# Optimization experiments

Measured on AMD Instinct MI355X. Metric: run time of the kernel, lower is better.

## Reference

```python
import jax, jax.numpy as jnp
import numpy as np

H = 2048      # hidden_size
DM = 4096     # intermediate_size
N = 16        # ssm state size
K = 4         # conv kernel
R = 128       # time_step_rank
B_SZ = 1
L = 1024


def setup_inputs() -> dict:
    key = jax.random.key(0)
    ks = jax.random.split(key, 10)
    s = 0.02
    hidden_states = jax.random.normal(ks[0], (B_SZ, L, H), dtype=jnp.float32)
    W_in = jax.random.normal(ks[1], (2 * DM, H), dtype=jnp.float32) * s
    conv_w = jax.random.normal(ks[2], (DM, 1, K), dtype=jnp.float32) * 0.3
    conv_b = jax.random.normal(ks[3], (DM,), dtype=jnp.float32) * 0.1
    W_x = jax.random.normal(ks[4], (R + 2 * N, DM), dtype=jnp.float32) * s
    W_dt = jax.random.normal(ks[5], (DM, R), dtype=jnp.float32) * s
    b_dt = jax.random.normal(ks[6], (DM,), dtype=jnp.float32) * 0.1
    # A_log init: log(arange(1..N)) broadcast over channels (per __init__)
    A_log = jnp.broadcast_to(jnp.log(jnp.arange(1, N + 1, dtype=jnp.float32))[None, :], (DM, N)).copy()
    D_param = jnp.ones((DM,), dtype=jnp.float32)
    W_out = jax.random.normal(ks[7], (H, DM), dtype=jnp.float32) * s
    return {"hidden_states": hidden_states, "W_in": W_in, "conv_w": conv_w,
            "conv_b": conv_b, "W_x": W_x, "W_dt": W_dt, "b_dt": b_dt,
            "A_log": A_log, "D_param": D_param, "W_out": W_out}


def reference(hidden_states, W_in, conv_w, conv_b, W_x, W_dt, b_dt, A_log, D_param, W_out):
    # in_proj then chunk into hidden / gate (torch chunks dim=1 after transpose)
    proj = hidden_states @ W_in.T                     # [B, L, 2D]
    h, gate = proj[..., :DM], proj[..., DM:]          # each [B, L, D]
    # depthwise causal conv1d, padding K-1 then truncate to L (left-pad == same)
    h_cl = jnp.transpose(h, (0, 2, 1))                # [B, D, L]
    hc = jax.lax.conv_general_dilated(
        h_cl, conv_w, window_strides=(1,), padding=[(K - 1, 0)],
        dimension_numbers=("NCH", "OIH", "NCH"), feature_group_count=DM)
    hc = jax.nn.silu(hc + conv_b[None, :, None])      # [B, D, L]
    hc_ld = jnp.transpose(hc, (0, 2, 1))              # [B, L, D]
    # x_proj -> dt, B, C
    ssm_p = hc_ld @ W_x.T                             # [B, L, R+2N]
    ts, Bm, Cm = ssm_p[..., :R], ssm_p[..., R:R + N], ssm_p[..., R + N:]
    dt = jax.nn.softplus(ts @ W_dt.T + b_dt)          # [B, L, D]
    A = -jnp.exp(A_log)                               # [D, N]
    dA = jnp.exp(dt[:, :, :, None] * A[None, None, :, :])            # [B, L, D, N]
    dBu = dt[:, :, :, None] * Bm[:, :, None, :] * hc_ld[:, :, :, None]  # [B, L, D, N]
    # selective scan over time: state = dA*state + dBu; y = <state, C>
    def step(state, inp):
        dA_t, dBu_t, C_t = inp                        # [B,D,N],[B,D,N],[B,N]
        state = dA_t * state + dBu_t
        y = jnp.einsum("bdn,bn->bd", state, C_t)
        return state, y
    init = jnp.zeros((hidden_states.shape[0], DM, N), dtype=hidden_states.dtype)
    _, ys = jax.lax.scan(step, init,
                         (jnp.swapaxes(dA, 0, 1), jnp.swapaxes(dBu, 0, 1), jnp.swapaxes(Cm, 0, 1)))
    y = jnp.transpose(ys, (1, 0, 2))                  # [B, L, D]
    y = y + hc_ld * D_param[None, None, :]            # skip via D
    y = y * jax.nn.silu(gate)                         # gating
    return y @ W_out.T                                # [B, L, H]
```

## Files before the change

### kernel.cpp

```cpp
#include <hip/hip_runtime.h>
#include <math.h>

#define AS1 __attribute__((address_space(1)))
#define AS3 __attribute__((address_space(3)))

typedef __attribute__((ext_vector_type(8))) short short8;
typedef __attribute__((ext_vector_type(4))) float f32x4;

static __device__ __forceinline__ unsigned short f2bf(float f) {
    unsigned u = __float_as_uint(f);
    unsigned r = (u + 0x7fffu + ((u >> 16) & 1u)) >> 16;
    return (unsigned short)r;
}

__global__ __launch_bounds__(256) void cvt_f32_bf16(const float* __restrict__ src,
                                                    unsigned short* __restrict__ dst,
                                                    int n4) {
    int i = blockIdx.x * 256 + threadIdx.x;
    int stride = gridDim.x * 256;
    for (; i < n4; i += stride) {
        float4 v = ((const float4*)src)[i];
        ushort4 o;
        o.x = f2bf(v.x); o.y = f2bf(v.y); o.z = f2bf(v.z); o.w = f2bf(v.w);
        ((ushort4*)dst)[i] = o;
    }
}

__global__ __launch_bounds__(256) void cvt_ts(const float* __restrict__ ssmp,
                                              unsigned short* __restrict__ ts) {
    int i = blockIdx.x * 256 + threadIdx.x;
    int t = i >> 5, c4 = (i & 31) * 4;
    float4 v = *(const float4*)&ssmp[t * 160 + c4];
    ushort4 o;
    o.x = f2bf(v.x); o.y = f2bf(v.y); o.z = f2bf(v.z); o.w = f2bf(v.w);
    *(ushort4*)&ts[t * 128 + c4] = o;
}

__global__ __launch_bounds__(256) void conv_silu(const float* __restrict__ h,
                                                 const float* __restrict__ cw,
                                                 const float* __restrict__ cb,
                                                 float* __restrict__ hc_f,
                                                 unsigned short* __restrict__ hc_bf) {
    int idx = blockIdx.x * 256 + threadIdx.x;
    int d = idx & 4095, t = idx >> 12;
    float acc = cb[d];
    float4 w = *(const float4*)&cw[d * 4];
    const float* wp = (const float*)&w;
#pragma unroll
    for (int k = 0; k < 4; ++k) {
        int tt = t + k - 3;
        if (tt >= 0) acc += h[tt * 4096 + d] * wp[k];
    }
    float s = acc / (1.f + __expf(-acc));
    hc_f[idx] = s;
    hc_bf[idx] = f2bf(s);
}

enum { EPI_PLAIN = 0, EPI_SPLIT = 1, EPI_ATOMIC = 2, EPI_SOFTPLUS = 3 };

template <int BM, int EPI>
__global__ __launch_bounds__(256)
void gemm_bt(const short* __restrict__ A, const short* __restrict__ B,
             float* __restrict__ C, float* __restrict__ C2,
             const float* __restrict__ bias,
             int M, int N, int K, int ldc, int kcLen) {
    __shared__ short A_lds[BM * 32];
    __shared__ short B_lds[128 * 32];
    const int tid = threadIdx.x;
    const int wv = tid >> 6, ln = tid & 63;
    const int lr = ln & 15, kg = ln >> 4;
    const int m0 = blockIdx.y * BM;
    const int n0 = blockIdx.x * 128;
    const int kbeg = blockIdx.z * kcLen;
    const int kend = kbeg + kcLen;
    const int wm = wv >> 1, wn = wv & 1;
    constexpr int MR = BM / 32;

    f32x4 acc[MR][4];
#pragma unroll
    for (int mi = 0; mi < MR; ++mi)
#pragma unroll
        for (int ni = 0; ni < 4; ++ni) acc[mi][ni] = (f32x4){0.f, 0.f, 0.f, 0.f};

    const int arow = tid >> 2;
    const int kq8 = (tid & 3) * 8;

    for (int k0 = kbeg; k0 < kend; k0 += 32) {
#pragma unroll
        for (int r = 0; r < BM / 64; ++r) {
            const short* srcA = A + (size_t)(m0 + r * 64 + arow) * K + (k0 + kq8);
            short* dstA = &A_lds[(r * 64 + wv * 16) * 32];
            __builtin_amdgcn_global_load_lds((const AS1 void*)srcA, (AS3 void*)dstA, 16, 0, 0);
        }
#pragma unroll
        for (int r = 0; r < 2; ++r) {
            int brow = n0 + r * 64 + arow;
            if (brow > N - 1) brow = N - 1;
            const short* srcB = B + (size_t)brow * K + (k0 + kq8);
            short* dstB = &B_lds[(r * 64 + wv * 16) * 32];
            __builtin_amdgcn_global_load_lds((const AS1 void*)srcB, (AS3 void*)dstB, 16, 0, 0);
        }
        __syncthreads();

        short8 av[MR], bv[4];
#pragma unroll
        for (int mi = 0; mi < MR; ++mi)
            av[mi] = *(const short8*)&A_lds[(wm * (BM / 2) + mi * 16 + lr) * 32 + kg * 8];
#pragma unroll
        for (int ni = 0; ni < 4; ++ni)
            bv[ni] = *(const short8*)&B_lds[(wn * 64 + ni * 16 + lr) * 32 + kg * 8];
#pragma unroll
        for (int mi = 0; mi < MR; ++mi)
#pragma unroll
            for (int ni = 0; ni < 4; ++ni)
                acc[mi][ni] = __builtin_amdgcn_mfma_f32_16x16x32_bf16(av[mi], bv[ni], acc[mi][ni], 0, 0, 0);
        __syncthreads();
    }

#pragma unroll
    for (int mi = 0; mi < MR; ++mi) {
        int crow0 = m0 + wm * (BM / 2) + mi * 16 + kg * 4;
#pragma unroll
        for (int ni = 0; ni < 4; ++ni) {
            int ccol = n0 + wn * 64 + ni * 16 + lr;
#pragma unroll
            for (int i = 0; i < 4; ++i) {
                float v = acc[mi][ni][i];
                size_t crow = (size_t)(crow0 + i);
                if constexpr (EPI == EPI_PLAIN) {
                    C[crow * ldc + ccol] = v;
                } else if constexpr (EPI == EPI_SPLIT) {
                    if (ccol < 4096) C[crow * 4096 + ccol] = v;
                    else C2[crow * 4096 + (ccol - 4096)] = v;
                } else if constexpr (EPI == EPI_ATOMIC) {
                    if (ccol < N) atomicAdd(&C[crow * ldc + ccol], v);
                } else {
                    float x = v + bias[ccol];
                    C[crow * ldc + ccol] = fmaxf(x, 0.f) + log1pf(__expf(-fabsf(x)));
                }
            }
        }
    }
}

#define CLEN 16
#define NCH 64

__global__ __launch_bounds__(256)
void scan_p1(const float* __restrict__ dt, const float* __restrict__ hc,
             const float* __restrict__ ssmp, const float* __restrict__ A_log,
             float* __restrict__ Sbuf, float* __restrict__ dtsum) {
    const int tid = threadIdx.x;
    const int c = blockIdx.x & (NCH - 1);
    const int db = blockIdx.x >> 6;
    const int d = db * 256 + tid;
    const int t0 = c * CLEN;

    float Ac[16];
#pragma unroll
    for (int i = 0; i < 4; ++i) {
        float4 v = *(const float4*)&A_log[d * 16 + i * 4];
        Ac[i*4+0] = -__expf(v.x); Ac[i*4+1] = -__expf(v.y);
        Ac[i*4+2] = -__expf(v.z); Ac[i*4+3] = -__expf(v.w);
    }

    __shared__ float sB[CLEN][16];
    sB[tid >> 4][tid & 15] = ssmp[(t0 + (tid >> 4)) * 160 + 128 + (tid & 15)];
    __syncthreads();

    float st[16];
#pragma unroll
    for (int n = 0; n < 16; ++n) st[n] = 0.f;
    float ds = 0.f;

    for (int tt = 0; tt < CLEN; ++tt) {
        float dtv = dt[(size_t)(t0 + tt) * 4096 + d];
        float hcv = hc[(size_t)(t0 + tt) * 4096 + d];
        float du = dtv * hcv;
        ds += dtv;
#pragma unroll
        for (int n = 0; n < 16; ++n) {
            float dA = __expf(dtv * Ac[n]);
            st[n] = fmaf(dA, st[n], du * sB[tt][n]);
        }
    }

    float* o = Sbuf + ((size_t)c * 4096 + d) * 16;
#pragma unroll
    for (int i = 0; i < 4; ++i)
        *(float4*)&o[i * 4] = make_float4(st[i*4], st[i*4+1], st[i*4+2], st[i*4+3]);
    dtsum[c * 4096 + d] = ds;
}

__global__ __launch_bounds__(256)
void scan_p2(const float* __restrict__ A_log, const float* __restrict__ dtsum,
             float* __restrict__ S) {
    const int idx = blockIdx.x * 256 + threadIdx.x;
    const int d = idx >> 4;
    const float Ac = -__expf(A_log[idx]);
    float s = 0.f;
    for (int c = 0; c < NCH; ++c) {
        size_t o = (size_t)c * 65536 + idx;
        float sl = S[o];
        float P = __expf(Ac * dtsum[c * 4096 + d]);
        S[o] = s;
        s = fmaf(P, s, sl);
    }
}

__global__ __launch_bounds__(256)
void scan_p3(const float* __restrict__ dt, const float* __restrict__ hc,
             const float* __restrict__ ssmp, const float* __restrict__ A_log,
             const float* __restrict__ Dp, const float* __restrict__ gate,
             const float* __restrict__ Sinit, unsigned short* __restrict__ y_bf) {
    const int tid = threadIdx.x;
    const int c = blockIdx.x & (NCH - 1);
    const int db = blockIdx.x >> 6;
    const int d = db * 256 + tid;
    const int t0 = c * CLEN;

    float Ac[16];
#pragma unroll
    for (int i = 0; i < 4; ++i) {
        float4 v = *(const float4*)&A_log[d * 16 + i * 4];
        Ac[i*4+0] = -__expf(v.x); Ac[i*4+1] = -__expf(v.y);
        Ac[i*4+2] = -__expf(v.z); Ac[i*4+3] = -__expf(v.w);
    }
    const float Dcoef = Dp[d];

    __shared__ float sB[CLEN][16], sC[CLEN][16];
    {
        int tt = tid >> 4, nn = tid & 15;
        sB[tt][nn] = ssmp[(t0 + tt) * 160 + 128 + nn];
        sC[tt][nn] = ssmp[(t0 + tt) * 160 + 144 + nn];
    }
    __syncthreads();

    float st[16];
    {
        const float* si = Sinit + ((size_t)c * 4096 + d) * 16;
#pragma unroll
        for (int i = 0; i < 4; ++i) {
            float4 v = *(const float4*)&si[i * 4];
            st[i*4] = v.x; st[i*4+1] = v.y; st[i*4+2] = v.z; st[i*4+3] = v.w;
        }
    }

    for (int tt = 0; tt < CLEN; ++tt) {
        size_t g = (size_t)(t0 + tt) * 4096 + d;
        float dtv = dt[g];
        float hcv = hc[g];
        float du = dtv * hcv;
        float p[16];
#pragma unroll
        for (int n = 0; n < 16; ++n) {
            float dA = __expf(dtv * Ac[n]);
            st[n] = fmaf(dA, st[n], du * sB[tt][n]);
            p[n] = st[n] * sC[tt][n];
        }
#pragma unroll
        for (int n = 0; n < 8; ++n) p[n] += p[n + 8];
#pragma unroll
        for (int n = 0; n < 4; ++n) p[n] += p[n + 4];
        p[0] += p[2]; p[1] += p[3];
        float csum = p[0] + p[1];
        float gv = gate[g];
        float yv = (csum + hcv * Dcoef) * (gv / (1.f + __expf(-gv)));
        y_bf[g] = f2bf(yv);
    }
}

extern "C" void kernel_launch(void* const* d_in, const int* in_sizes, int n_in,
                              void* d_out, int out_size, void* d_ws, size_t ws_size,
                              hipStream_t stream) {
    (void)in_sizes; (void)n_in; (void)out_size; (void)ws_size;
    const float* hidden = (const float*)d_in[0];
    const float* W_in   = (const float*)d_in[1];
    const float* conv_w = (const float*)d_in[2];
    const float* conv_b = (const float*)d_in[3];
    const float* W_x    = (const float*)d_in[4];
    const float* W_dt   = (const float*)d_in[5];
    const float* b_dt   = (const float*)d_in[6];
    const float* A_log  = (const float*)d_in[7];
    const float* D_p    = (const float*)d_in[8];
    const float* W_out  = (const float*)d_in[9];
    float* out = (float*)d_out;

    char* w = (char*)d_ws;
    unsigned short* hid_bf = (unsigned short*)w;  w += (size_t)1024 * 2048 * 2;
    unsigned short* Wbig   = (unsigned short*)w;  w += (size_t)8192 * 2048 * 2;
    float* h_buf           = (float*)w;           w += (size_t)1024 * 4096 * 4;
    float* gate            = (float*)w;           w += (size_t)1024 * 4096 * 4;
    float* hc_f            = (float*)w;           w += (size_t)1024 * 4096 * 4;
    unsigned short* hc_bf  = (unsigned short*)w;  w += (size_t)1024 * 4096 * 2;
    float* ssmp            = (float*)w;           w += (size_t)1024 * 160 * 4;
    unsigned short* ts_bf  = (unsigned short*)w;  w += (size_t)1024 * 128 * 2;
    unsigned short* Wx_bf  = (unsigned short*)w;  w += (size_t)160 * 4096 * 2;
    unsigned short* Wdt_bf = (unsigned short*)w;  w += (size_t)4096 * 128 * 2;
    unsigned short* y_bf   = (unsigned short*)w;  w += (size_t)1024 * 4096 * 2;
    float* Sbuf            = (float*)w;           w += (size_t)NCH * 4096 * 16 * 4;
    float* dtsum           = (float*)w;           w += (size_t)NCH * 4096 * 4;

    hipMemsetAsync(ssmp, 0, (size_t)1024 * 160 * 4, stream);

    cvt_f32_bf16<<<2048, 256, 0, stream>>>(hidden, hid_bf, 1024 * 2048 / 4);
    cvt_f32_bf16<<<4096, 256, 0, stream>>>(W_in, Wbig, 8192 * 2048 / 4);
    cvt_f32_bf16<<<640, 256, 0, stream>>>(W_x, Wx_bf, 160 * 4096 / 4);
    cvt_f32_bf16<<<512, 256, 0, stream>>>(W_dt, Wdt_bf, 4096 * 128 / 4);

    gemm_bt<128, EPI_SPLIT><<<dim3(64, 8, 1), 256, 0, stream>>>(
        (const short*)hid_bf, (const short*)Wbig, h_buf, gate, nullptr,
        1024, 8192, 2048, 8192, 2048);

    conv_silu<<<16384, 256, 0, stream>>>(h_buf, conv_w, conv_b, hc_f, hc_bf);

    cvt_f32_bf16<<<2048, 256, 0, stream>>>(W_out, Wbig, 2048 * 4096 / 4);

    gemm_bt<128, EPI_ATOMIC><<<dim3(2, 8, 16), 256, 0, stream>>>(
        (const short*)hc_bf, (const short*)Wx_bf, ssmp, nullptr, nullptr,
        1024, 160, 4096, 160, 256);

    cvt_ts<<<128, 256, 0, stream>>>(ssmp, ts_bf);

    gemm_bt<128, EPI_SOFTPLUS><<<dim3(32, 8, 1), 256, 0, stream>>>(
        (const short*)ts_bf, (const short*)Wdt_bf, h_buf, nullptr, b_dt,
        1024, 4096, 128, 4096, 128);

    scan_p1<<<NCH * 16, 256, 0, stream>>>(h_buf, hc_f, ssmp, A_log, Sbuf, dtsum);
    scan_p2<<<256, 256, 0, stream>>>(A_log, dtsum, Sbuf);
    scan_p3<<<NCH * 16, 256, 0, stream>>>(h_buf, hc_f, ssmp, A_log, D_p, gate, Sbuf, y_bf);

    gemm_bt<64, EPI_PLAIN><<<dim3(16, 16, 1), 256, 0, stream>>>(
        (const short*)y_bf, (const short*)Wbig, out, nullptr, nullptr,
        1024, 2048, 4096, 2048, 4096);
}
```

Baseline: 269.7 us.

## Replace in_proj GEMM with 512-thread 128x256 tile double-buffered LDS kernel

Swaps the in_proj GEMM for a new kernel that uses 8 waves per block, a 128x256 output tile with BK=64, and async global_load_lds into double-buffered, XOR-swizzled LDS. Block IDs are remapped so neighbouring blocks share panels in L2. The aim is more operand reuse per block and overlapping global loads with MFMA work. In exchange it needs more LDS and registers, allowing at most 2 blocks per CU, and an unused three-stage variant is left in the file.

Measured after the change: 252.0 us. -6.5%, faster.

```diff
diff --git a/kernel.cpp b/kernel.cpp
--- a/kernel.cpp
+++ b/kernel.cpp
@@ -6,6 +6,9 @@
 
 typedef __attribute__((ext_vector_type(8))) short short8;
 typedef __attribute__((ext_vector_type(4))) float f32x4;
+
+#define WAITV(n) asm volatile("s_waitcnt vmcnt(" #n ")" ::: "memory")
+#define BARRIER() asm volatile("s_barrier" ::: "memory")
 
 static __device__ __forceinline__ unsigned short f2bf(float f) {
     unsigned u = __float_as_uint(f);
@@ -54,6 +57,224 @@
     float s = acc / (1.f + __expf(-acc));
     hc_f[idx] = s;
     hc_bf[idx] = f2bf(s);
+}
+
+__global__ __launch_bounds__(512, 2)
+void gemm8p_split(const short* __restrict__ A, const short* __restrict__ B,
+                  float* __restrict__ C0, float* __restrict__ C1,
+                  int M, int N, int K) {
+    __shared__ short lds[2 * 24576];
+
+    const int tid = threadIdx.x;
+    const int wv = tid >> 6, ln = tid & 63;
+    const int lr = ln & 15, kg = ln >> 4;
+    const int wm = wv >> 2, wn = wv & 3;
+
+    const int bid = blockIdx.x;
+    const int swz = (bid & 7) * 32 + (bid >> 3);
+    const int by = swz & 7, bx = swz >> 3;
+    const int m0 = by * 128;
+    const int n0 = bx * 256;
+    const int NT = K >> 6;
+
+    f32x4 acc[4][4];
+#pragma unroll
+    for (int mi = 0; mi < 4; ++mi)
+#pragma unroll
+        for (int ni = 0; ni < 4; ++ni) acc[mi][ni] = (f32x4){0.f, 0.f, 0.f, 0.f};
+
+    const short* Abase = A + (size_t)m0 * K;
+    const short* Bbase = B + (size_t)n0 * K;
+
+#define STAGE(kt, b)                                                          \
+    {                                                                         \
+        short* lbase = &lds[(b) * 24576];                                     \
+        _Pragma("unroll")                                                     \
+        for (int r = 0; r < 2; ++r) {                                         \
+            int c = r * 512 + tid;                                            \
+            int row = c >> 3, cb8 = (c & 7) << 4;                             \
+            int scb = cb8 ^ ((row & 7) << 4);                                 \
+            const short* src = Abase + (size_t)row * K + (kt) * 64 + (scb >> 1); \
+            short* dst = lbase + (r * 512 + wv * 64) * 8;                     \
+            __builtin_amdgcn_global_load_lds((const AS1 void*)src,            \
+                                             (AS3 void*)dst, 16, 0, 0);       \
+        }                                                                     \
+        _Pragma("unroll")                                                     \
+        for (int r = 0; r < 4; ++r) {                                         \
+            int c = r * 512 + tid;                                            \
+            int row = c >> 3, cb8 = (c & 7) << 4;                             \
+            int scb = cb8 ^ ((row & 7) << 4);                                 \
+            const short* src = Bbase + (size_t)row * K + (kt) * 64 + (scb >> 1); \
+            short* dst = lbase + 8192 + (r * 512 + wv * 64) * 8;              \
+            __builtin_amdgcn_global_load_lds((const AS1 void*)src,            \
+                                             (AS3 void*)dst, 16, 0, 0);       \
+        }                                                                     \
+    }
+
+    STAGE(0, 0);
+    if (NT > 1) STAGE(1, 1);
+
+    for (int kt = 0; kt < NT; ++kt) {
+        const int b = kt & 1;
+        if (kt + 2 < NT) STAGE(kt + 2, b);
+        if (kt + 1 < NT) { WAITV(6); } else { WAITV(0); }
+        BARRIER();
+        {
+            const short* la = &lds[b * 24576];
+            const short* lb = la + 8192;
+#pragma unroll
+            for (int ks = 0; ks < 2; ++ks) {
+                short8 av[4], bv[4];
+#pragma unroll
+                for (int mi = 0; mi < 4; ++mi) {
+                    int row = wm * 64 + mi * 16 + lr;
+                    int col = (ks * 32 + kg * 8) ^ ((row & 7) << 3);
+                    av[mi] = *(const short8*)&la[row * 64 + col];
+                }
+#pragma unroll
+                for (int ni = 0; ni < 4; ++ni) {
+                    int row = wn * 64 + ni * 16 + lr;
+                    int col = (ks * 32 + kg * 8) ^ ((row & 7) << 3);
+                    bv[ni] = *(const short8*)&lb[row * 64 + col];
+                }
+                __builtin_amdgcn_s_setprio(1);
+#pragma unroll
+                for (int mi = 0; mi < 4; ++mi)
+#pragma unroll
+                    for (int ni = 0; ni < 4; ++ni)
+                        acc[mi][ni] = __builtin_amdgcn_mfma_f32_16x16x32_bf16(
+                            av[mi], bv[ni], acc[mi][ni], 0, 0, 0);
+                __builtin_amdgcn_s_setprio(0);
+            }
+        }
+        BARRIER();
+    }
+#undef STAGE
+
+#pragma unroll
+    for (int mi = 0; mi < 4; ++mi) {
+        int crow0 = m0 + wm * 64 + mi * 16 + kg * 4;
+#pragma unroll
+        for (int ni = 0; ni < 4; ++ni) {
+            int ccol = n0 + wn * 64 + ni * 16 + lr;
+#pragma unroll
+            for (int i = 0; i < 4; ++i) {
+                float v = acc[mi][ni][i];
+                size_t crow = (size_t)(crow0 + i);
+                if (ccol < 4096) C0[crow * 4096 + ccol] = v;
+                else C1[crow * 4096 + (ccol - 4096)] = v;
+            }
+        }
+    }
+}
+
+
+__global__ __launch_bounds__(512, 2)
+void gemm8p_split_v2(const short* __restrict__ A, const short* __restrict__ B,
+                     float* __restrict__ C0, float* __restrict__ C1,
+                     int M, int N, int K) {
+    __shared__ short lds[2 * 24576];
+
+    const int tid = threadIdx.x;
+    const int wv = tid >> 6, ln = tid & 63;
+    const int lr = ln & 15, kg = ln >> 4;
+    const int wm = wv >> 2, wn = wv & 3;
+
+    const int bid = blockIdx.x;
+    const int swz = (bid & 7) * 32 + (bid >> 3);
+    const int by = swz & 7, bx = swz >> 3;
+    const int m0 = by * 128;
+    const int n0 = bx * 256;
+    const int NT = K >> 6;
+
+    f32x4 acc[4][4];
+#pragma unroll
+    for (int mi = 0; mi < 4; ++mi)
+#pragma unroll
+        for (int ni = 0; ni < 4; ++ni) acc[mi][ni] = (f32x4){0.f, 0.f, 0.f, 0.f};
+
+    const short* Abase = A + (size_t)m0 * K;
+    const short* Bbase = B + (size_t)n0 * K;
+
+#define STAGE(kt, b)                                                          \
+    {                                                                         \
+        short* lbase = &lds[(b) * 24576];                                     \
+        _Pragma("unroll")                                                     \
+        for (int r = 0; r < 2; ++r) {                                         \
+            int c = r * 512 + tid;                                            \
+            int row = c >> 3, cb8 = (c & 7) << 4;                             \
+            int scb = cb8 ^ ((row & 7) << 4);                                 \
+            const short* src = Abase + (size_t)row * K + (kt) * 64 + (scb >> 1); \
+            short* dst = lbase + (r * 512 + wv * 64) * 8;                     \
+            __builtin_amdgcn_global_load_lds((const AS1 void*)src,            \
+                                             (AS3 void*)dst, 16, 0, 0);       \
+        }                                                                     \
+        _Pragma("unroll")                                                     \
+        for (int r = 0; r < 4; ++r) {                                         \
+            int c = r * 512 + tid;                                            \
+            int row = c >> 3, cb8 = (c & 7) << 4;                             \
+            int scb = cb8 ^ ((row & 7) << 4);                                 \
+            const short* src = Bbase + (size_t)row * K + (kt) * 64 + (scb >> 1); \
+            short* dst = lbase + 8192 + (r * 512 + wv * 64) * 8;              \
+            __builtin_amdgcn_global_load_lds((const AS1 void*)src,            \
+                                             (AS3 void*)dst, 16, 0, 0);       \
+        }                                                                     \
+    }
+
+    STAGE(0, 0);
+
+    for (int kt = 0; kt < NT; ++kt) {
+        const int b = kt & 1;
+        if (kt + 1 < NT) STAGE(kt + 1, b ^ 1);
+        if (kt + 1 < NT) { WAITV(6); } else { WAITV(0); }
+        BARRIER();
+        {
+            const short* la = &lds[b * 24576];
+            const short* lb = la + 8192;
+#pragma unroll
+            for (int ks = 0; ks < 2; ++ks) {
+                short8 av[4], bv[4];
+#pragma unroll
+                for (int mi = 0; mi < 4; ++mi) {
+                    int row = wm * 64 + mi * 16 + lr;
+                    int col = (ks * 32 + kg * 8) ^ ((row & 7) << 3);
+                    av[mi] = *(const short8*)&la[row * 64 + col];
+                }
+#pragma unroll
+                for (int ni = 0; ni < 4; ++ni) {
+                    int row = wn * 64 + ni * 16 + lr;
+                    int col = (ks * 32 + kg * 8) ^ ((row & 7) << 3);
+                    bv[ni] = *(const short8*)&lb[row * 64 + col];
+                }
+                __builtin_amdgcn_s_setprio(1);
+#pragma unroll
+                for (int mi = 0; mi < 4; ++mi)
+#pragma unroll
+                    for (int ni = 0; ni < 4; ++ni)
+                        acc[mi][ni] = __builtin_amdgcn_mfma_f32_16x16x32_bf16(
+                            av[mi], bv[ni], acc[mi][ni], 0, 0, 0);
+                __builtin_amdgcn_s_setprio(0);
+            }
+        }
+        BARRIER();
+    }
+#undef STAGE
+
+#pragma unroll
+    for (int mi = 0; mi < 4; ++mi) {
+        int crow0 = m0 + wm * 64 + mi * 16 + kg * 4;
+#pragma unroll
+        for (int ni = 0; ni < 4; ++ni) {
+            int ccol = n0 + wn * 64 + ni * 16 + lr;
+#pragma unroll
+            for (int i = 0; i < 4; ++i) {
+                float v = acc[mi][ni][i];
+                size_t crow = (size_t)(crow0 + i);
+                if (ccol < 4096) C0[crow * 4096 + ccol] = v;
+                else C1[crow * 4096 + (ccol - 4096)] = v;
+            }
+        }
+    }
 }
 
 enum { EPI_PLAIN = 0, EPI_SPLIT = 1, EPI_ATOMIC = 2, EPI_SOFTPLUS = 3 };
@@ -308,9 +529,8 @@
     cvt_f32_bf16<<<640, 256, 0, stream>>>(W_x, Wx_bf, 160 * 4096 / 4);
     cvt_f32_bf16<<<512, 256, 0, stream>>>(W_dt, Wdt_bf, 4096 * 128 / 4);
 
-    gemm_bt<128, EPI_SPLIT><<<dim3(64, 8, 1), 256, 0, stream>>>(
-        (const short*)hid_bf, (const short*)Wbig, h_buf, gate, nullptr,
-        1024, 8192, 2048, 8192, 2048);
+    gemm8p_split_v2<<<256, 512, 0, stream>>>(
+        (const short*)hid_bf, (const short*)Wbig, h_buf, gate, 1024, 8192, 2048);
 
     conv_silu<<<16384, 256, 0, stream>>>(h_buf, conv_w, conv_b, hc_f, hc_bf);
 
```

## Add 512-thread double-buffered direct-to-LDS GEMM for in_proj and out_proj

Applied to the files above, without the earlier changes.

Adds a new bf16 MFMA GEMM kernel with 128x256 tiles, 8 waves, and a K-step of 64. It double-buffers global_load_lds with an XOR-swizzled LDS layout and a swizzled block order, and uses the new kernel for the large in_proj and out_proj GEMMs. The out_proj now runs split-K over 4 chunks with atomic adds into a zero-initialised output, which adds a memset and atomic traffic in exchange for more workgroups. The aim is higher MFMA utilisation and better L2 reuse than the older 256-thread gemm_bt.

Result: faster. 236.3 us (-12.4%).

```diff
diff --git a/kernel.cpp b/kernel.cpp
--- a/kernel.cpp
+++ b/kernel.cpp
@@ -6,6 +6,9 @@
 
 typedef __attribute__((ext_vector_type(8))) short short8;
 typedef __attribute__((ext_vector_type(4))) float f32x4;
+
+#define WAITV(n) asm volatile("s_waitcnt vmcnt(" #n ")" ::: "memory")
+#define BARRIER() asm volatile("s_barrier" ::: "memory")
 
 static __device__ __forceinline__ unsigned short f2bf(float f) {
     unsigned u = __float_as_uint(f);
@@ -54,6 +57,123 @@
     float s = acc / (1.f + __expf(-acc));
     hc_f[idx] = s;
     hc_bf[idx] = f2bf(s);
+}
+
+enum { P_SPLIT = 0, P_ATOMIC = 1 };
+
+template <int EPI>
+__global__ __launch_bounds__(512, 2)
+void gemm8p(const short* __restrict__ A, const short* __restrict__ B,
+            float* __restrict__ C0, float* __restrict__ C1,
+            int N, int K, int kchunk) {
+    __shared__ short lds[2 * 24576];
+
+    const int tid = threadIdx.x;
+    const int wv = tid >> 6, ln = tid & 63;
+    const int lr = ln & 15, kg = ln >> 4;
+    const int wm = wv >> 2, wn = wv & 3;
+
+    const int nwg = gridDim.x;
+    const int bid = blockIdx.x;
+    const int swz = (bid & 7) * (nwg >> 3) + (bid >> 3);
+    const int by = swz & 7, bx = swz >> 3;
+    const int m0 = by * 128;
+    const int n0 = bx * 256;
+    const int kbeg = blockIdx.z * kchunk;
+    const int NT = kchunk >> 6;
+
+    f32x4 acc[4][4];
+#pragma unroll
+    for (int mi = 0; mi < 4; ++mi)
+#pragma unroll
+        for (int ni = 0; ni < 4; ++ni) acc[mi][ni] = (f32x4){0.f, 0.f, 0.f, 0.f};
+
+    const short* Abase = A + (size_t)m0 * K + kbeg;
+    const short* Bbase = B + (size_t)n0 * K + kbeg;
+
+#define STAGE(kt, b)                                                          \
+    {                                                                         \
+        short* lbase = &lds[(b) * 24576];                                     \
+        _Pragma("unroll")                                                     \
+        for (int r = 0; r < 2; ++r) {                                         \
+            int c = r * 512 + tid;                                            \
+            int row = c >> 3, cb8 = (c & 7) << 4;                             \
+            int scb = cb8 ^ ((row & 7) << 4);                                 \
+            const short* src = Abase + (size_t)row * K + (kt) * 64 + (scb >> 1); \
+            short* dst = lbase + (r * 512 + wv * 64) * 8;                     \
+            __builtin_amdgcn_global_load_lds((const AS1 void*)src,            \
+                                             (AS3 void*)dst, 16, 0, 0);       \
+        }                                                                     \
+        _Pragma("unroll")                                                     \
+        for (int r = 0; r < 4; ++r) {                                         \
+            int c = r * 512 + tid;                                            \
+            int row = c >> 3, cb8 = (c & 7) << 4;                             \
+            int scb = cb8 ^ ((row & 7) << 4);                                 \
+            const short* src = Bbase + (size_t)row * K + (kt) * 64 + (scb >> 1); \
+            short* dst = lbase + 8192 + (r * 512 + wv * 64) * 8;              \
+            __builtin_amdgcn_global_load_lds((const AS1 void*)src,            \
+                                             (AS3 void*)dst, 16, 0, 0);       \
+        }                                                                     \
+    }
+
+    STAGE(0, 0);
+
+    for (int kt = 0; kt < NT; ++kt) {
+        const int b = kt & 1;
+        if (kt + 1 < NT) STAGE(kt + 1, b ^ 1);
+        if (kt + 1 < NT) { WAITV(6); } else { WAITV(0); }
+        BARRIER();
+        {
+            const short* la = &lds[b * 24576];
+            const short* lb = la + 8192;
+#pragma unroll
+            for (int ks = 0; ks < 2; ++ks) {
+                short8 av[4], bv[4];
+#pragma unroll
+                for (int mi = 0; mi < 4; ++mi) {
+                    int row = wm * 64 + mi * 16 + lr;
+                    int col = (ks * 32 + kg * 8) ^ ((row & 7) << 3);
+                    av[mi] = *(const short8*)&la[row * 64 + col];
+                }
+#pragma unroll
+                for (int ni = 0; ni < 4; ++ni) {
+                    int row = wn * 64 + ni * 16 + lr;
+                    int col = (ks * 32 + kg * 8) ^ ((row & 7) << 3);
+                    bv[ni] = *(const short8*)&lb[row * 64 + col];
+                }
+                __builtin_amdgcn_s_setprio(1);
+#pragma unroll
+                for (int mi = 0; mi < 4; ++mi)
+#pragma unroll
+                    for (int ni = 0; ni < 4; ++ni)
+                        acc[mi][ni] = __builtin_amdgcn_mfma_f32_16x16x32_bf16(
+                            av[mi], bv[ni], acc[mi][ni], 0, 0, 0);
+                __builtin_amdgcn_s_setprio(0);
+            }
+        }
+        BARRIER();
+    }
+#undef STAGE
+
+#pragma unroll
+    for (int mi = 0; mi < 4; ++mi) {
+        int crow0 = m0 + wm * 64 + mi * 16 + kg * 4;
+#pragma unroll
+        for (int ni = 0; ni < 4; ++ni) {
+            int ccol = n0 + wn * 64 + ni * 16 + lr;
+#pragma unroll
+            for (int i = 0; i < 4; ++i) {
+                float v = acc[mi][ni][i];
+                size_t crow = (size_t)(crow0 + i);
+                if constexpr (EPI == P_SPLIT) {
+                    if (ccol < 4096) C0[crow * 4096 + ccol] = v;
+                    else C1[crow * 4096 + (ccol - 4096)] = v;
+                } else {
+                    atomicAdd(&C0[crow * N + ccol], v);
+                }
+            }
+        }
+    }
 }
 
 enum { EPI_PLAIN = 0, EPI_SPLIT = 1, EPI_ATOMIC = 2, EPI_SOFTPLUS = 3 };
@@ -302,15 +422,15 @@
     float* dtsum           = (float*)w;           w += (size_t)NCH * 4096 * 4;
 
     hipMemsetAsync(ssmp, 0, (size_t)1024 * 160 * 4, stream);
+    hipMemsetAsync(out, 0, (size_t)1024 * 2048 * 4, stream);
 
     cvt_f32_bf16<<<2048, 256, 0, stream>>>(hidden, hid_bf, 1024 * 2048 / 4);
     cvt_f32_bf16<<<4096, 256, 0, stream>>>(W_in, Wbig, 8192 * 2048 / 4);
     cvt_f32_bf16<<<640, 256, 0, stream>>>(W_x, Wx_bf, 160 * 4096 / 4);
     cvt_f32_bf16<<<512, 256, 0, stream>>>(W_dt, Wdt_bf, 4096 * 128 / 4);
 
-    gemm_bt<128, EPI_SPLIT><<<dim3(64, 8, 1), 256, 0, stream>>>(
-        (const short*)hid_bf, (const short*)Wbig, h_buf, gate, nullptr,
-        1024, 8192, 2048, 8192, 2048);
+    gemm8p<P_SPLIT><<<dim3(256, 1, 1), 512, 0, stream>>>(
+        (const short*)hid_bf, (const short*)Wbig, h_buf, gate, 8192, 2048, 2048);
 
     conv_silu<<<16384, 256, 0, stream>>>(h_buf, conv_w, conv_b, hc_f, hc_bf);
 
@@ -330,7 +450,6 @@
     scan_p2<<<256, 256, 0, stream>>>(A_log, dtsum, Sbuf);
     scan_p3<<<NCH * 16, 256, 0, stream>>>(h_buf, hc_f, ssmp, A_log, D_p, gate, Sbuf, y_bf);
 
-    gemm_bt<64, EPI_PLAIN><<<dim3(16, 16, 1), 256, 0, stream>>>(
-        (const short*)y_bf, (const short*)Wbig, out, nullptr, nullptr,
-        1024, 2048, 4096, 2048, 4096);
-}
+    gemm8p<P_ATOMIC><<<dim3(64, 1, 4), 512, 0, stream>>>(
+        (const short*)y_bf, (const short*)Wbig, out, nullptr, 2048, 4096, 1024);
+}
```
